# Performance work log

Measured on AMD Instinct MI355X. Metric: run time of the kernel, lower is better.

## Reference

```python
import jax, jax.numpy as jnp
import numpy as np

N_NODES = 100000


def _mean_aggregate(feat, src, dst, num_nodes):
    # mean over edges (src -> dst) of feat[src], grouped by dst; 0 for isolated nodes
    summed = jax.ops.segment_sum(feat[src], dst, num_segments=num_nodes)  # [N, d]
    deg = jax.ops.segment_sum(jnp.ones((src.shape[0],), feat.dtype), dst,
                              num_segments=num_nodes)  # [N]
    return summed / jnp.maximum(deg, 1.0)[:, None]


def setup_inputs() -> dict:
    key = jax.random.key(0)
    k1, k2, k3 = jax.random.split(key, 3)
    feat = jax.random.normal(k1, (N_NODES, 128), dtype=jnp.float32)
    # fc_self_neigh weight: Linear(3*in_feats=384 -> out_feats=128), no bias
    W = jax.random.normal(k2, (128, 384), dtype=jnp.float32) * 0.05
    edge_index = jax.random.randint(k3, (2, 800000), 0, N_NODES, dtype=jnp.int32)
    return {"feat": feat, "W": W, "edge_index": edge_index}


def reference(feat, W, edge_index):
    src, dst = edge_index[0], edge_index[1]
    n = feat.shape[0]
    h_self = feat  # feat_drop = 0.0
    # forward SAGE: mean of in-neighbor (source) features per destination node
    fwd_neigh = _mean_aggregate(feat, src, dst, n)
    # backward SAGE on reversed graph: mean of out-neighbor (dest) features per source node
    bwd_neigh = _mean_aggregate(feat, dst, src, n)
    h = jnp.concatenate((h_self, fwd_neigh, bwd_neigh), axis=1)  # [N, 3*d]
    rst = h @ W.T  # [N, out_feats], bias=False
    return jax.nn.relu(rst)
```

## Files before the change

kernel.cpp:

```cpp
#include <hip/hip_runtime.h>
#include <hip/hip_bf16.h>

#define D 128
#define CHUNK 1024
#define NXCD 8

typedef __attribute__((ext_vector_type(8))) short bf16x8;
typedef __attribute__((ext_vector_type(4))) float f32x4;

__device__ inline float bflo(unsigned u) { return __uint_as_float(u << 16); }
__device__ inline float bfhi(unsigned u) { return __uint_as_float(u & 0xffff0000u); }
__device__ inline unsigned short f2bf(float f) {
    __hip_bfloat16 h = __float2bfloat16(f);
    return *reinterpret_cast<unsigned short*>(&h);
}
__device__ inline unsigned pack2bf(float lo, float hi) {
    return (unsigned)f2bf(lo) | ((unsigned)f2bf(hi) << 16);
}

__global__ __launch_bounds__(256) void prep_kernel(
    const float* __restrict__ feat, unsigned short* __restrict__ featb, int n4f,
    const float* __restrict__ W, unsigned short* __restrict__ Wb, int n4w,
    const int* __restrict__ src, const int* __restrict__ dst,
    int* __restrict__ cnt, int E, int N)
{
    int i = blockIdx.x * blockDim.x + threadIdx.x;
    const int stride = gridDim.x * blockDim.x;
    const int total = n4f + n4w + E;
    for (; i < total; i += stride) {
        if (i < n4f + n4w) {
            const float* x; unsigned short* y; int j;
            if (i < n4f) { x = feat; y = featb; j = i; }
            else         { x = W;    y = Wb;    j = i - n4f; }
            float4 v = *reinterpret_cast<const float4*>(&x[(size_t)j * 4]);
            uint2 o;
            o.x = pack2bf(v.x, v.y);
            o.y = pack2bf(v.z, v.w);
            *reinterpret_cast<uint2*>(&y[(size_t)j * 4]) = o;
        } else {
            const int e = i - n4f - n4w;
            atomicAdd(&cnt[dst[e]], 1);
            atomicAdd(&cnt[N + src[e]], 1);
        }
    }
}

__global__ __launch_bounds__(256) void scan1_kernel(
    const int* __restrict__ cnt, int* __restrict__ blk, int n2)
{
    __shared__ int red[256];
    const int b = blockIdx.x, t = threadIdx.x;
    const int base = b * CHUNK + t * 4;
    int s = 0;
    if (base + 3 < n2) {
        int4 v = *reinterpret_cast<const int4*>(&cnt[base]);
        s = v.x + v.y + v.z + v.w;
    } else {
        for (int j = 0; j < 4; ++j) { int idx = base + j; if (idx < n2) s += cnt[idx]; }
    }
    red[t] = s; __syncthreads();
    for (int o = 128; o > 0; o >>= 1) { if (t < o) red[t] += red[t + o]; __syncthreads(); }
    if (t == 0) blk[b] = red[0];
}

__global__ __launch_bounds__(256) void scan2_kernel(int* __restrict__ blk, int NB)
{
    __shared__ int sh[256];
    const int t = threadIdx.x;
    sh[t] = (t < NB) ? blk[t] : 0;
    __syncthreads();
    for (int o = 1; o < 256; o <<= 1) {
        int v = (t >= o) ? sh[t - o] : 0;
        __syncthreads();
        sh[t] += v;
        __syncthreads();
    }
    if (t < NB) blk[t] = (t > 0) ? sh[t - 1] : 0;
}

__global__ __launch_bounds__(256) void scan3_kernel(
    const int* __restrict__ cnt, const int* __restrict__ blk,
    int* __restrict__ off, int* __restrict__ cur, int n2, int total)
{
    __shared__ int sh[256];
    const int b = blockIdx.x, t = threadIdx.x;
    const int base = b * CHUNK + t * 4;
    int v[4]; int s = 0;
    for (int j = 0; j < 4; ++j) { int idx = base + j; v[j] = (idx < n2) ? cnt[idx] : 0; s += v[j]; }
    sh[t] = s; __syncthreads();
    for (int o = 1; o < 256; o <<= 1) {
        int x = (t >= o) ? sh[t - o] : 0;
        __syncthreads();
        sh[t] += x;
        __syncthreads();
    }
    int excl = blk[b] + ((t > 0) ? sh[t - 1] : 0);
    for (int j = 0; j < 4; ++j) {
        int idx = base + j;
        if (idx < n2) { off[idx] = excl; cur[idx] = excl; }
        excl += v[j];
    }
    if (b == 0 && t == 0) off[n2] = total;
}

__global__ __launch_bounds__(256) void scatter_ids_kernel(
    const int* __restrict__ src, const int* __restrict__ dst,
    int* __restrict__ cur, int* __restrict__ csr,
    int E, int N, int npr)
{
    const int grp = blockIdx.x & (NXCD - 1);
    const int bIn = blockIdx.x >> 3;
    const int nbk = gridDim.x >> 3;
    const int lo = grp * npr;
    const int hi = lo + npr;

    int i = bIn * 256 + threadIdx.x;
    const int stride = nbk * 256;
    for (int e = i; e < E; e += stride) {
        const int s = src[e];
        const int d = dst[e];
        if (d >= lo && d < hi) {
            int p = atomicAdd(&cur[d], 1);
            csr[p] = s;
        }
        if (s >= lo && s < hi) {
            int p2 = atomicAdd(&cur[N + s], 1);
            csr[p2] = d;
        }
    }
}

__global__ __launch_bounds__(256) void gather_mean_kernel(
    const unsigned short* __restrict__ featb, const int* __restrict__ off,
    const int* __restrict__ csr, unsigned short* __restrict__ meanb, int n2)
{
    const int tid = blockIdx.x * 256 + threadIdx.x;
    const int seg = tid >> 4;
    const int l = tid & 15;
    if (seg >= n2) return;

    const int beg = off[seg], end = off[seg + 1];
    float a0=0,a1=0,a2=0,a3=0,a4=0,a5=0,a6=0,a7=0;

    int e = beg;
    for (; e + 3 < end; e += 4) {
        const int n0 = csr[e], n1 = csr[e + 1], n2i = csr[e + 2], n3 = csr[e + 3];
        const uint4 v0 = *reinterpret_cast<const uint4*>(featb + (size_t)n0 * D + l * 8);
        const uint4 v1 = *reinterpret_cast<const uint4*>(featb + (size_t)n1 * D + l * 8);
        const uint4 v2 = *reinterpret_cast<const uint4*>(featb + (size_t)n2i * D + l * 8);
        const uint4 v3 = *reinterpret_cast<const uint4*>(featb + (size_t)n3 * D + l * 8);
        a0 += (bflo(v0.x) + bflo(v1.x)) + (bflo(v2.x) + bflo(v3.x));
        a1 += (bfhi(v0.x) + bfhi(v1.x)) + (bfhi(v2.x) + bfhi(v3.x));
        a2 += (bflo(v0.y) + bflo(v1.y)) + (bflo(v2.y) + bflo(v3.y));
        a3 += (bfhi(v0.y) + bfhi(v1.y)) + (bfhi(v2.y) + bfhi(v3.y));
        a4 += (bflo(v0.z) + bflo(v1.z)) + (bflo(v2.z) + bflo(v3.z));
        a5 += (bfhi(v0.z) + bfhi(v1.z)) + (bfhi(v2.z) + bfhi(v3.z));
        a6 += (bflo(v0.w) + bflo(v1.w)) + (bflo(v2.w) + bflo(v3.w));
        a7 += (bfhi(v0.w) + bfhi(v1.w)) + (bfhi(v2.w) + bfhi(v3.w));
    }
    for (; e < end; ++e) {
        const int n0 = csr[e];
        const uint4 v0 = *reinterpret_cast<const uint4*>(featb + (size_t)n0 * D + l * 8);
        a0 += bflo(v0.x); a1 += bfhi(v0.x);
        a2 += bflo(v0.y); a3 += bfhi(v0.y);
        a4 += bflo(v0.z); a5 += bfhi(v0.z);
        a6 += bflo(v0.w); a7 += bfhi(v0.w);
    }

    const int deg = end - beg;
    const float inv = 1.0f / (float)((deg > 1) ? deg : 1);
    uint4 o;
    o.x = pack2bf(a0 * inv, a1 * inv);
    o.y = pack2bf(a2 * inv, a3 * inv);
    o.z = pack2bf(a4 * inv, a5 * inv);
    o.w = pack2bf(a6 * inv, a7 * inv);
    *reinterpret_cast<uint4*>(meanb + (size_t)seg * D + l * 8) = o;
}

__global__ __launch_bounds__(512) void mfma_gemm_kernel(
    const unsigned short* __restrict__ featb,
    const unsigned short* __restrict__ meanb,
    const unsigned short* __restrict__ Wb,
    float* __restrict__ out, int N)
{
    __shared__ unsigned short wlds[2][128 * 128];

    const int t = threadIdx.x;
    const int wv = t >> 6;
    const int lane = t & 63;
    const int r = lane & 15;
    const int q = lane >> 4;

    const int row0 = blockIdx.x * 128 + wv * 16;
    const int row = row0 + r;
    const int rowc = (row < N) ? row : (N - 1);

    const unsigned short* h0 = featb + (size_t)rowc * D;
    const unsigned short* h1 = meanb + (size_t)rowc * D;
    const unsigned short* h2 = meanb + ((size_t)N + rowc) * D;
    bf16x8 af[12];
#pragma unroll
    for (int kk = 0; kk < 4; ++kk) {
        af[kk]     = *reinterpret_cast<const bf16x8*>(h0 + kk * 32 + q * 8);
        af[4 + kk] = *reinterpret_cast<const bf16x8*>(h1 + kk * 32 + q * 8);
        af[8 + kk] = *reinterpret_cast<const bf16x8*>(h2 + kk * 32 + q * 8);
    }

    const int sc = t >> 2;
    const int sq = t & 3;
    const char* wsrc = reinterpret_cast<const char*>(Wb) + (size_t)sc * 768;
    const int swz = (sc & 7) << 4;

    f32x4 acc[8];
#pragma unroll
    for (int n = 0; n < 8; ++n) acc[n] = (f32x4){0.f, 0.f, 0.f, 0.f};

    {
        uint4 st[4];
#pragma unroll
        for (int j = 0; j < 4; ++j)
            st[j] = *reinterpret_cast<const uint4*>(wsrc + j * 64 + sq * 16);
        char* wb0 = reinterpret_cast<char*>(&wlds[0][0]) + sc * 256;
#pragma unroll
        for (int j = 0; j < 4; ++j)
            *reinterpret_cast<uint4*>(wb0 + ((j * 64 + sq * 16) ^ swz)) = st[j];
    }
    __syncthreads();

#pragma unroll
    for (int ci = 0; ci < 3; ++ci) {
        uint4 nx[4];
        if (ci < 2) {
#pragma unroll
            for (int j = 0; j < 4; ++j)
                nx[j] = *reinterpret_cast<const uint4*>(
                    wsrc + (ci + 1) * 256 + j * 64 + sq * 16);
        }

        const char* wl = reinterpret_cast<const char*>(&wlds[ci & 1][0]);
#pragma unroll
        for (int kk = 0; kk < 4; ++kk) {
            const bf16x8 bh = af[ci * 4 + kk];
#pragma unroll
            for (int n = 0; n < 8; ++n) {
                const int c = n * 16 + r;
                const bf16x8 aw = *reinterpret_cast<const bf16x8*>(
                    wl + c * 256 + ((kk * 64 + q * 16) ^ ((c & 7) << 4)));
                acc[n] = __builtin_amdgcn_mfma_f32_16x16x32_bf16(aw, bh, acc[n], 0, 0, 0);
            }
        }

        if (ci < 2) {
            char* wbn = reinterpret_cast<char*>(&wlds[(ci + 1) & 1][0]) + sc * 256;
#pragma unroll
            for (int j = 0; j < 4; ++j)
                *reinterpret_cast<uint4*>(wbn + ((j * 64 + sq * 16) ^ swz)) = nx[j];
            __syncthreads();
        }
    }

    if (row < N) {
        float* orow = out + (size_t)row * D;
#pragma unroll
        for (int n = 0; n < 8; ++n) {
            float4 v;
            v.x = fmaxf(acc[n][0], 0.0f);
            v.y = fmaxf(acc[n][1], 0.0f);
            v.z = fmaxf(acc[n][2], 0.0f);
            v.w = fmaxf(acc[n][3], 0.0f);
            *reinterpret_cast<float4*>(orow + n * 16 + q * 4) = v;
        }
    }
}

extern "C" void kernel_launch(void* const* d_in, const int* in_sizes, int n_in,
                              void* d_out, int out_size, void* d_ws, size_t ws_size,
                              hipStream_t stream) {
    const float* feat = (const float*)d_in[0];
    const float* W    = (const float*)d_in[1];
    const int*   ei   = (const int*)d_in[2];
    float*       out  = (float*)d_out;

    const int E = in_sizes[2] / 2;
    const int N = in_sizes[0] / D;
    const int n2 = 2 * N;
    const int* src = ei;
    const int* dst = ei + E;

    int* cnt = (int*)d_ws;
    int* cur = cnt + n2;
    int* off = cur + n2;
    int* blk = off + (n2 + 4);
    int* csr = blk + 256;
    unsigned short* featb = (unsigned short*)(csr + 2 * E);
    unsigned short* Wb    = featb + (size_t)N * D;
    unsigned short* meanb = Wb + 128 * 384;

    hipMemsetAsync(cnt, 0, (size_t)n2 * sizeof(int), stream);

    const int NB = (n2 + CHUNK - 1) / CHUNK;
    const int npr = (N + NXCD - 1) / NXCD;
    const int n4f = N * D / 4;
    const int n4w = 128 * 384 / 4;

    prep_kernel<<<2048, 256, 0, stream>>>(feat, featb, n4f, W, Wb, n4w,
                                          src, dst, cnt, E, N);

    scan1_kernel<<<NB, 256, 0, stream>>>(cnt, blk, n2);
    scan2_kernel<<<1, 256, 0, stream>>>(blk, NB);
    scan3_kernel<<<NB, 256, 0, stream>>>(cnt, blk, off, cur, n2, 2 * E);
    scatter_ids_kernel<<<2048, 256, 0, stream>>>(src, dst, cur, csr, E, N, npr);

    const int gather_blocks = (n2 * 16 + 255) / 256;
    gather_mean_kernel<<<gather_blocks, 256, 0, stream>>>(featb, off, csr, meanb, n2);

    mfma_gemm_kernel<<<(N + 127) / 128, 512, 0, stream>>>(featb, meanb, Wb, out, N);
}
```

Baseline: 267.3 us.

## Record per-edge ranks during counting; drop scatter atomics and fold scan2 into scan3

The counting pass now stores the value returned by each atomicAdd as that edge's rank within its segment. The scatter pass then writes to off[seg]+rank directly, with no second round of atomics and no cur array. The small block-prefix scan kernel is merged into scan3, where every block redundantly scans the block sums, which removes one launch. The cost is two extra E-sized rank arrays written and then re-read, which adds memory traffic in place of atomic contention.

```diff
diff --git a/kernel.cpp b/kernel.cpp
--- a/kernel.cpp
+++ b/kernel.cpp
@@ -22,7 +22,8 @@
     const float* __restrict__ feat, unsigned short* __restrict__ featb, int n4f,
     const float* __restrict__ W, unsigned short* __restrict__ Wb, int n4w,
     const int* __restrict__ src, const int* __restrict__ dst,
-    int* __restrict__ cnt, int E, int N)
+    int* __restrict__ cnt, int* __restrict__ rankF, int* __restrict__ rankB,
+    int E, int N)
 {
     int i = blockIdx.x * blockDim.x + threadIdx.x;
     const int stride = gridDim.x * blockDim.x;
@@ -39,8 +40,8 @@
             *reinterpret_cast<uint2*>(&y[(size_t)j * 4]) = o;
         } else {
             const int e = i - n4f - n4w;
-            atomicAdd(&cnt[dst[e]], 1);
-            atomicAdd(&cnt[N + src[e]], 1);
+            rankF[e] = atomicAdd(&cnt[dst[e]], 1);
+            rankB[e] = atomicAdd(&cnt[N + src[e]], 1);
         }
     }
 }
@@ -63,27 +64,24 @@
     if (t == 0) blk[b] = red[0];
 }
 
-__global__ __launch_bounds__(256) void scan2_kernel(int* __restrict__ blk, int NB)
+__global__ __launch_bounds__(256) void scan3_kernel(
+    const int* __restrict__ cnt, const int* __restrict__ blk,
+    int* __restrict__ off, int n2, int total, int NB)
 {
     __shared__ int sh[256];
-    const int t = threadIdx.x;
-    sh[t] = (t < NB) ? blk[t] : 0;
+    __shared__ int bs[256];
+    const int b = blockIdx.x, t = threadIdx.x;
+
+    bs[t] = (t < NB) ? blk[t] : 0;
     __syncthreads();
     for (int o = 1; o < 256; o <<= 1) {
-        int v = (t >= o) ? sh[t - o] : 0;
+        int v = (t >= o) ? bs[t - o] : 0;
         __syncthreads();
-        sh[t] += v;
+        bs[t] += v;
         __syncthreads();
     }
-    if (t < NB) blk[t] = (t > 0) ? sh[t - 1] : 0;
-}
-
-__global__ __launch_bounds__(256) void scan3_kernel(
-    const int* __restrict__ cnt, const int* __restrict__ blk,
-    int* __restrict__ off, int* __restrict__ cur, int n2, int total)
-{
-    __shared__ int sh[256];
-    const int b = blockIdx.x, t = threadIdx.x;
+    const int blkpref = (b > 0) ? bs[b - 1] : 0;
+
     const int base = b * CHUNK + t * 4;
     int v[4]; int s = 0;
     for (int j = 0; j < 4; ++j) { int idx = base + j; v[j] = (idx < n2) ? cnt[idx] : 0; s += v[j]; }
@@ -94,10 +92,10 @@
         sh[t] += x;
         __syncthreads();
     }
-    int excl = blk[b] + ((t > 0) ? sh[t - 1] : 0);
+    int excl = blkpref + ((t > 0) ? sh[t - 1] : 0);
     for (int j = 0; j < 4; ++j) {
         int idx = base + j;
-        if (idx < n2) { off[idx] = excl; cur[idx] = excl; }
+        if (idx < n2) off[idx] = excl;
         excl += v[j];
     }
     if (b == 0 && t == 0) off[n2] = total;
@@ -105,8 +103,9 @@
 
 __global__ __launch_bounds__(256) void scatter_ids_kernel(
     const int* __restrict__ src, const int* __restrict__ dst,
-    int* __restrict__ cur, int* __restrict__ csr,
-    int E, int N, int npr)
+    const int* __restrict__ off,
+    const int* __restrict__ rankF, const int* __restrict__ rankB,
+    int* __restrict__ csr, int E, int N, int npr)
 {
     const int grp = blockIdx.x & (NXCD - 1);
     const int bIn = blockIdx.x >> 3;
@@ -120,12 +119,10 @@
         const int s = src[e];
         const int d = dst[e];
         if (d >= lo && d < hi) {
-            int p = atomicAdd(&cur[d], 1);
-            csr[p] = s;
+            csr[off[d] + rankF[e]] = s;
         }
         if (s >= lo && s < hi) {
-            int p2 = atomicAdd(&cur[N + s], 1);
-            csr[p2] = d;
+            csr[off[N + s] + rankB[e]] = d;
         }
     }
 }
@@ -287,11 +284,12 @@
     const int* src = ei;
     const int* dst = ei + E;
 
-    int* cnt = (int*)d_ws;
-    int* cur = cnt + n2;
-    int* off = cur + n2;
-    int* blk = off + (n2 + 4);
-    int* csr = blk + 256;
+    int* cnt   = (int*)d_ws;
+    int* off   = cnt + n2;
+    int* blk   = off + (n2 + 4);
+    int* rankF = blk + 256;
+    int* rankB = rankF + E;
+    int* csr   = rankB + E;
     unsigned short* featb = (unsigned short*)(csr + 2 * E);
     unsigned short* Wb    = featb + (size_t)N * D;
     unsigned short* meanb = Wb + 128 * 384;
@@ -304,12 +302,12 @@
     const int n4w = 128 * 384 / 4;
 
     prep_kernel<<<2048, 256, 0, stream>>>(feat, featb, n4f, W, Wb, n4w,
-                                          src, dst, cnt, E, N);
+                                          src, dst, cnt, rankF, rankB, E, N);
 
     scan1_kernel<<<NB, 256, 0, stream>>>(cnt, blk, n2);
-    scan2_kernel<<<1, 256, 0, stream>>>(blk, NB);
-    scan3_kernel<<<NB, 256, 0, stream>>>(cnt, blk, off, cur, n2, 2 * E);
-    scatter_ids_kernel<<<2048, 256, 0, stream>>>(src, dst, cur, csr, E, N, npr);
+    scan3_kernel<<<NB, 256, 0, stream>>>(cnt, blk, off, n2, 2 * E, NB);
+    scatter_ids_kernel<<<2048, 256, 0, stream>>>(src, dst, off, rankF, rankB,
+                                                 csr, E, N, npr);
 
     const int gather_blocks = (n2 * 16 + 255) / 256;
     gather_mean_kernel<<<gather_blocks, 256, 0, stream>>>(featb, off, csr, meanb, n2);
```

New measurement: 238.5 us. 1.12x faster.
